# Kernel optimization log

Hardware: AMD Instinct MI355X
Metric: run time of the kernel (lower is better)

Reference implementation:

```python
import jax, jax.numpy as jnp
import numpy as np

IN_SIZE = 96
HIDDEN = 128
LIN_IN = 32
T = 65536


def setup_inputs() -> dict:
    key = jax.random.key(0)
    ks = jax.random.split(key, 6)
    s_ih = 1.0 / np.sqrt(HIDDEN)
    return {
        "input_GRU": jax.random.normal(ks[0], (T, IN_SIZE), dtype=jnp.float32),
        "input_linear": jax.random.normal(ks[1], (T, LIN_IN), dtype=jnp.float32),
        "init_hidden": jnp.zeros((HIDDEN,), dtype=jnp.float32),
        "w_ih": (jax.random.normal(ks[2], (3 * HIDDEN, IN_SIZE), dtype=jnp.float32) * s_ih),
        "w_hh": (jax.random.normal(ks[3], (3 * HIDDEN, HIDDEN), dtype=jnp.float32) * s_ih),
        "b_ih": (jax.random.normal(ks[4], (3 * HIDDEN,), dtype=jnp.float32) * s_ih),
        "b_n": (jax.random.normal(ks[5], (HIDDEN,), dtype=jnp.float32) * s_ih),
        "lin_bias": jnp.zeros((1,), dtype=jnp.float32),
    }


def reference(input_GRU, input_linear, init_hidden, w_ih, w_hh, b_ih, b_n, lin_bias):
    # Precompute all input-to-hidden projections as one big GEMM: (T, 3H)
    igates_all = input_GRU @ w_ih.T + b_ih

    def step(h, inp):
        igates, x_lin = inp
        hgates = w_hh @ h  # (3H,)
        ir, iz, in_ = jnp.split(igates, 3)
        hr, hz, hn = jnp.split(hgates, 3)
        r = jax.nn.sigmoid(ir + hr)  # reset gate
        z = jax.nn.sigmoid(iz + hz)  # update gate
        n = jnp.tanh(in_ + r * (hn + b_n))  # candidate
        h_new = n + z * (h - n)  # equinox GRUCell update
        # dynamic linear readout: first LIN_IN hidden units act as weight row
        out = jnp.dot(h_new[:LIN_IN], x_lin)[None] + lin_bias  # (1,)
        return h_new, out

    _, out = jax.lax.scan(step, init_hidden, (igates_all, input_linear))
    return out  # (T, 1)
```

## Files before the change

### kernel.cpp

```cpp
#include <hip/hip_runtime.h>
#include <math.h>

#define IN_SIZE 96
#define HID 128
#define H3 384
#define LIN_IN 32

__global__ __launch_bounds__(384, 2)
void igates_kernel(const float* __restrict__ x, const float* __restrict__ w_ih,
                   const float* __restrict__ b_ih, float* __restrict__ ig, int T)
{
    const int TT = 16;
    int t0 = blockIdx.x * TT;
    int j = threadIdx.x;
    __shared__ __align__(16) float xs[TT * IN_SIZE];
    for (int idx = j; idx < TT * IN_SIZE; idx += H3)
        xs[idx] = x[(size_t)t0 * IN_SIZE + idx];
    __syncthreads();

    float acc[TT];
    float b = b_ih[j];
#pragma unroll
    for (int tt = 0; tt < TT; tt++) acc[tt] = b;

    const float4* w4 = (const float4*)(w_ih + (size_t)j * IN_SIZE);
#pragma unroll
    for (int k = 0; k < IN_SIZE / 4; k++) {
        float4 wv = w4[k];
#pragma unroll
        for (int tt = 0; tt < TT; tt++) {
            const float4* xv4 = (const float4*)(xs + tt * IN_SIZE);
            float4 xv = xv4[k];
            acc[tt] = fmaf(wv.x, xv.x, acc[tt]);
            acc[tt] = fmaf(wv.y, xv.y, acc[tt]);
            acc[tt] = fmaf(wv.z, xv.z, acc[tt]);
            acc[tt] = fmaf(wv.w, xv.w, acc[tt]);
        }
    }
#pragma unroll
    for (int tt = 0; tt < TT; tt++)
        ig[(size_t)(t0 + tt) * H3 + j] = acc[tt];
}

__device__ __forceinline__ void fma4(float4& acc, const float4& wv, const float4& hv)
{
    acc.x = fmaf(wv.x, hv.x, acc.x);
    acc.y = fmaf(wv.y, hv.y, acc.y);
    acc.z = fmaf(wv.z, hv.z, acc.z);
    acc.w = fmaf(wv.w, hv.w, acc.w);
}

__device__ __forceinline__ float quad_sum(float x)
{
    float t;
    t = __int_as_float(__builtin_amdgcn_mov_dpp(__float_as_int(x), 0xB1, 0xF, 0xF, true));
    x += t;
    t = __int_as_float(__builtin_amdgcn_mov_dpp(__float_as_int(x), 0x4E, 0xF, 0xF, true));
    x += t;
    return x;
}

__device__ __forceinline__ void fast_barrier()
{
    asm volatile("s_waitcnt lgkmcnt(0)\n\ts_barrier" ::: "memory");
}

#define HPAD 36

__global__ __launch_bounds__(512, 2)
void scan_kernel(const float* __restrict__ ig, const float* __restrict__ h0,
                 const float* __restrict__ w_hh, const float* __restrict__ b_n,
                 float* __restrict__ hlin, int T)
{
    __shared__ __align__(16) float hs[4 * HPAD];

    const int tid = threadIdx.x;
    const int j = tid >> 2;
    const int kseg = tid & 3;
    const bool gate_lane = (kseg == 0);

    float4 w0[8], w1[8], w2[8];
    {
        const float* b0 = w_hh + (size_t)j * HID + kseg * 32;
        const float* b1 = w_hh + (size_t)(j + HID) * HID + kseg * 32;
        const float* b2 = w_hh + (size_t)(j + 2 * HID) * HID + kseg * 32;
#pragma unroll
        for (int k = 0; k < 8; k++) {
            w0[k] = ((const float4*)b0)[k];
            w1[k] = ((const float4*)b1)[k];
            w2[k] = ((const float4*)b2)[k];
        }
    }
    if (tid < HID) hs[(tid >> 5) * HPAD + (tid & 31)] = h0[tid];

    float bn = 0.f;
    float p00 = 0.f, p01 = 0.f, p02 = 0.f;
    float p10 = 0.f, p11 = 0.f, p12 = 0.f;
    if (gate_lane) {
        bn = b_n[j];
        p00 = ig[j];
        p01 = ig[HID + j];
        p02 = ig[2 * HID + j];
        const float* q = ig + H3;
        p10 = q[j];
        p11 = q[HID + j];
        p12 = q[2 * HID + j];
    }
    __syncthreads();

    const float4* hp = (const float4*)(hs + kseg * HPAD);
    const int hwidx = (j >> 5) * HPAD + (j & 31);

    const float* pf = ig + (size_t)2 * H3 + j;
    float* hl = hlin + j;

#define MATVEC_GATES(C0, C1, C2, DO_PREFETCH)                                  \
    {                                                                          \
        float4 a0 = {0.f, 0.f, 0.f, 0.f}, a1 = a0, a2 = a0;                    \
        _Pragma("unroll")                                                      \
        for (int kk = 0; kk < 8; kk++) {                                       \
            float4 hv = hp[kk];                                                \
            fma4(a0, w0[kk], hv);                                              \
            fma4(a1, w1[kk], hv);                                              \
            fma4(a2, w2[kk], hv);                                              \
        }                                                                      \
        float s0 = (a0.x + a0.y) + (a0.z + a0.w);                              \
        float s1 = (a1.x + a1.y) + (a1.z + a1.w);                              \
        float s2 = (a2.x + a2.y) + (a2.z + a2.w);                              \
        s0 = quad_sum(s0); s1 = quad_sum(s1); s2 = quad_sum(s2);               \
        if (gate_lane) {                                                       \
            float hprev = hs[hwidx];                                           \
            float er = __expf(-(C0 + s0));                                     \
            float r = __builtin_amdgcn_rcpf(1.f + er);                         \
            float ez = __expf(-(C1 + s1));                                     \
            float z = __builtin_amdgcn_rcpf(1.f + ez);                         \
            float xn = C2 + r * (s2 + bn);                                     \
            float e2 = __expf(-2.f * fabsf(xn));                               \
            float th = (1.f - e2) * __builtin_amdgcn_rcpf(1.f + e2);           \
            float nn = copysignf(th, xn);                                      \
            float hnew = nn + z * (hprev - nn);                                \
            hs[hwidx] = hnew;                                                  \
            if (j < LIN_IN) *hl = hnew;                                        \
            if (DO_PREFETCH) {                 \
                C0 = pf[0];                                                    \
                C1 = pf[HID];                                                  \
                C2 = pf[2 * HID];                                              \
            }                                                                  \
        }                                                                      \
        hl += LIN_IN;                                                          \
        pf += H3;                                                              \
        fast_barrier();                                                        \
    }

    int s = 0;
    for (; s + 4 <= T; s += 2) {
        MATVEC_GATES(p00, p01, p02, true)
        MATVEC_GATES(p10, p11, p12, true)
    }
    MATVEC_GATES(p00, p01, p02, false)
    MATVEC_GATES(p10, p11, p12, false)
#undef MATVEC_GATES
}

__global__ __launch_bounds__(256)
void readout_kernel(const float* __restrict__ hlin, const float* __restrict__ xlin,
                    const float* __restrict__ lbias, float* __restrict__ out, int T)
{
    int gid = blockIdx.x * 256 + threadIdx.x;
    int t = gid >> 3;
    int seg = gid & 7;
    if (t < T) {
        float4 hv = ((const float4*)hlin)[(size_t)t * 8 + seg];
        float4 xv = ((const float4*)xlin)[(size_t)t * 8 + seg];
        float p = hv.x * xv.x + hv.y * xv.y + hv.z * xv.z + hv.w * xv.w;
        p += __shfl_xor(p, 1);
        p += __shfl_xor(p, 2);
        p += __shfl_xor(p, 4);
        if (seg == 0) out[t] = p + lbias[0];
    }
}

extern "C" void kernel_launch(void* const* d_in, const int* in_sizes, int n_in,
                              void* d_out, int out_size, void* d_ws, size_t ws_size,
                              hipStream_t stream) {
    const float* x_gru = (const float*)d_in[0];
    const float* x_lin = (const float*)d_in[1];
    const float* h0    = (const float*)d_in[2];
    const float* w_ih  = (const float*)d_in[3];
    const float* w_hh  = (const float*)d_in[4];
    const float* b_ih  = (const float*)d_in[5];
    const float* b_n   = (const float*)d_in[6];
    const float* lbias = (const float*)d_in[7];
    float* out = (float*)d_out;

    int T = in_sizes[0] / IN_SIZE;
    float* igates = (float*)d_ws;
    float* hlin   = (float*)d_ws + (size_t)T * H3;

    igates_kernel<<<T / 16, 384, 0, stream>>>(x_gru, w_ih, b_ih, igates, T);
    scan_kernel<<<1, 512, 0, stream>>>(igates, h0, w_hh, b_n, hlin, T);
    readout_kernel<<<(T * 8 + 255) / 256, 256, 0, stream>>>(hlin, x_lin, lbias, out, T);
}
```

Baseline: 32.01 ms.

## Split recurrent matvec across 768 threads with shared-memory gate exchange

The scan kernel now assigns each thread pair one row of w_hh (split in K halves) across 768 threads, instead of 512 threads each holding three gate rows for a quarter of K. Gate pre-activations are written to shared memory and the first 128 threads apply the GRU update after an extra barrier. This shortens each thread's serial FMA chain and removes the DPP reduction stages, at the cost of a second barrier per timestep and an extra shared-memory round trip on the serial critical path.

After: 60.76 ms. 1.9x slower.

```diff
diff --git a/kernel.cpp b/kernel.cpp
--- a/kernel.cpp
+++ b/kernel.cpp
@@ -50,14 +50,11 @@
     acc.w = fmaf(wv.w, hv.w, acc.w);
 }
 
-__device__ __forceinline__ float quad_sum(float x)
+__device__ __forceinline__ float dpp_xor1_add(float x)
 {
-    float t;
-    t = __int_as_float(__builtin_amdgcn_mov_dpp(__float_as_int(x), 0xB1, 0xF, 0xF, true));
-    x += t;
-    t = __int_as_float(__builtin_amdgcn_mov_dpp(__float_as_int(x), 0x4E, 0xF, 0xF, true));
-    x += t;
-    return x;
+    float t = __int_as_float(
+        __builtin_amdgcn_mov_dpp(__float_as_int(x), 0xB1, 0xF, 0xF, true));
+    return x + t;
 }
 
 __device__ __forceinline__ void fast_barrier()
@@ -65,101 +62,97 @@
     asm volatile("s_waitcnt lgkmcnt(0)\n\ts_barrier" ::: "memory");
 }
 
-#define HPAD 36
+__device__ __forceinline__ float gru_gate(float c0, float c1, float c2,
+                                          float s0, float s1, float s2,
+                                          float bn, float hprev)
+{
+    float er = __expf(-(c0 + s0));
+    float r = __builtin_amdgcn_rcpf(1.f + er);
+    float ez = __expf(-(c1 + s1));
+    float z = __builtin_amdgcn_rcpf(1.f + ez);
+    float xn = c2 + r * (s2 + bn);
+    float e2 = __expf(-2.f * fabsf(xn));
+    float th = (1.f - e2) * __builtin_amdgcn_rcpf(1.f + e2);
+    float nn = copysignf(th, xn);
+    return nn + z * (hprev - nn);
+}
 
-__global__ __launch_bounds__(512, 2)
+__global__ __launch_bounds__(768, 3)
 void scan_kernel(const float* __restrict__ ig, const float* __restrict__ h0,
                  const float* __restrict__ w_hh, const float* __restrict__ b_n,
                  float* __restrict__ hlin, int T)
 {
-    __shared__ __align__(16) float hs[4 * HPAD];
+    __shared__ __align__(16) float hs[HID];
+    __shared__ float hg[H3];
 
     const int tid = threadIdx.x;
-    const int j = tid >> 2;
-    const int kseg = tid & 3;
-    const bool gate_lane = (kseg == 0);
+    const int row = tid >> 1;
+    const int khalf = tid & 1;
 
-    float4 w0[8], w1[8], w2[8];
+    float4 w[16];
     {
-        const float* b0 = w_hh + (size_t)j * HID + kseg * 32;
-        const float* b1 = w_hh + (size_t)(j + HID) * HID + kseg * 32;
-        const float* b2 = w_hh + (size_t)(j + 2 * HID) * HID + kseg * 32;
+        const float4* wb = (const float4*)(w_hh + (size_t)row * HID + khalf * 64);
 #pragma unroll
-        for (int k = 0; k < 8; k++) {
-            w0[k] = ((const float4*)b0)[k];
-            w1[k] = ((const float4*)b1)[k];
-            w2[k] = ((const float4*)b2)[k];
-        }
+        for (int k = 0; k < 16; k++) w[k] = wb[k];
     }
-    if (tid < HID) hs[(tid >> 5) * HPAD + (tid & 31)] = h0[tid];
+    if (tid < HID) hs[tid] = h0[tid];
 
     float bn = 0.f;
     float p00 = 0.f, p01 = 0.f, p02 = 0.f;
     float p10 = 0.f, p11 = 0.f, p12 = 0.f;
-    if (gate_lane) {
-        bn = b_n[j];
-        p00 = ig[j];
-        p01 = ig[HID + j];
-        p02 = ig[2 * HID + j];
+    const float* pf = ig + (size_t)2 * H3 + tid;
+    float* hl = hlin + tid;
+    if (tid < HID) {
+        bn = b_n[tid];
+        p00 = ig[tid];
+        p01 = ig[HID + tid];
+        p02 = ig[2 * HID + tid];
         const float* q = ig + H3;
-        p10 = q[j];
-        p11 = q[HID + j];
-        p12 = q[2 * HID + j];
+        p10 = q[tid];
+        p11 = q[HID + tid];
+        p12 = q[2 * HID + tid];
     }
     __syncthreads();
 
-    const float4* hp = (const float4*)(hs + kseg * HPAD);
-    const int hwidx = (j >> 5) * HPAD + (j & 31);
+    const float4* hp = (const float4*)hs + khalf * 16;
 
-    const float* pf = ig + (size_t)2 * H3 + j;
-    float* hl = hlin + j;
-
-#define MATVEC_GATES(C0, C1, C2, DO_PREFETCH)                                  \
+#define STEP(C0, C1, C2, DO_PREFETCH)                                          \
     {                                                                          \
-        float4 a0 = {0.f, 0.f, 0.f, 0.f}, a1 = a0, a2 = a0;                    \
+        float4 acc = {0.f, 0.f, 0.f, 0.f};                                     \
         _Pragma("unroll")                                                      \
-        for (int kk = 0; kk < 8; kk++) {                                       \
-            float4 hv = hp[kk];                                                \
-            fma4(a0, w0[kk], hv);                                              \
-            fma4(a1, w1[kk], hv);                                              \
-            fma4(a2, w2[kk], hv);                                              \
-        }                                                                      \
-        float s0 = (a0.x + a0.y) + (a0.z + a0.w);                              \
-        float s1 = (a1.x + a1.y) + (a1.z + a1.w);                              \
-        float s2 = (a2.x + a2.y) + (a2.z + a2.w);                              \
-        s0 = quad_sum(s0); s1 = quad_sum(s1); s2 = quad_sum(s2);               \
-        if (gate_lane) {                                                       \
-            float hprev = hs[hwidx];                                           \
-            float er = __expf(-(C0 + s0));                                     \
-            float r = __builtin_amdgcn_rcpf(1.f + er);                         \
-            float ez = __expf(-(C1 + s1));                                     \
-            float z = __builtin_amdgcn_rcpf(1.f + ez);                         \
-            float xn = C2 + r * (s2 + bn);                                     \
-            float e2 = __expf(-2.f * fabsf(xn));                               \
-            float th = (1.f - e2) * __builtin_amdgcn_rcpf(1.f + e2);           \
-            float nn = copysignf(th, xn);                                      \
-            float hnew = nn + z * (hprev - nn);                                \
-            hs[hwidx] = hnew;                                                  \
-            if (j < LIN_IN) *hl = hnew;                                        \
+        for (int kk = 0; kk < 16; kk++)                                        \
+            fma4(acc, w[kk], hp[kk]);                                          \
+        float s = (acc.x + acc.y) + (acc.z + acc.w);                           \
+        s = dpp_xor1_add(s);             \
+        if (khalf == 0) hg[row] = s;                                           \
+        fast_barrier();                                                        \
+        if (tid < HID) {                     \
+            float hr = hg[tid];                                                \
+            float hz = hg[HID + tid];                                          \
+            float hn = hg[2 * HID + tid];                                      \
+            float hprev = hs[tid];                                             \
+            float hnew = gru_gate(C0, C1, C2, hr, hz, hn, bn, hprev);          \
+            hs[tid] = hnew;                                                    \
+            if (tid < LIN_IN) *hl = hnew;                                      \
             if (DO_PREFETCH) {                 \
                 C0 = pf[0];                                                    \
                 C1 = pf[HID];                                                  \
                 C2 = pf[2 * HID];                                              \
             }                                                                  \
+            hl += LIN_IN;                                                      \
+            pf += H3;                                                          \
         }                                                                      \
-        hl += LIN_IN;                                                          \
-        pf += H3;                                                              \
         fast_barrier();                                                        \
     }
 
     int s = 0;
     for (; s + 4 <= T; s += 2) {
-        MATVEC_GATES(p00, p01, p02, true)
-        MATVEC_GATES(p10, p11, p12, true)
+        STEP(p00, p01, p02, true)
+        STEP(p10, p11, p12, true)
     }
-    MATVEC_GATES(p00, p01, p02, false)
-    MATVEC_GATES(p10, p11, p12, false)
-#undef MATVEC_GATES
+    STEP(p00, p01, p02, false)
+    STEP(p10, p11, p12, false)
+#undef STEP
 }
 
 __global__ __launch_bounds__(256)
@@ -198,6 +191,6 @@
     float* hlin   = (float*)d_ws + (size_t)T * H3;
 
     igates_kernel<<<T / 16, 384, 0, stream>>>(x_gru, w_ih, b_ih, igates, T);
-    scan_kernel<<<1, 512, 0, stream>>>(igates, h0, w_hh, b_n, hlin, T);
+    scan_kernel<<<1, 768, 0, stream>>>(igates, h0, w_hh, b_n, hlin, T);
     readout_kernel<<<(T * 8 + 255) / 256, 256, 0, stream>>>(hlin, x_lin, lbias, out, T);
 }
```
